# Kernel tuning notes

Hardware: AMD Instinct MI355X
Metric: run time of the kernel (lower is better)

The kernel has to match this reference:

```python
import jax, jax.numpy as jnp
import numpy as np

E = 8          # moe_expert_count
CAPACITY = 1024  # per-expert capacity C = S / E (capacity factor 1)


def _top1_gate(features, wg):
    """Top-1 gate with capacity, returning combine_weights [S,E,C],
    dispatch_mask [S,E,C], and load-balancing aux loss (standard Switch/BASE-style gate
    matching the (l_aux, combine_weights, dispatch_mask) interface used by BaseLayer)."""
    S, M = features.shape
    logits = features @ wg                      # [S, E]
    gates = jax.nn.softmax(logits, axis=-1)     # [S, E]
    idx = jnp.argmax(gates, axis=-1)            # [S] expert assignment
    mask1 = jax.nn.one_hot(idx, E, dtype=features.dtype)  # [S, E]
    # position of each token inside its expert's buffer (0-based, order of arrival)
    locations = jnp.cumsum(mask1, axis=0) - mask1          # [S, E]
    loc = jnp.sum(locations * mask1, axis=1).astype(jnp.int32)  # [S]
    keep = (loc < CAPACITY).astype(features.dtype)          # drop overflow tokens
    mask1 = mask1 * keep[:, None]
    gate_s = jnp.sum(gates * mask1, axis=1)                 # [S] gate prob of kept tokens
    loc_oh = jax.nn.one_hot(loc, CAPACITY, dtype=features.dtype)  # [S, C]
    combine = gate_s[:, None, None] * mask1[:, :, None] * loc_oh[:, None, :]  # [S,E,C]
    dispatch = (combine > 0).astype(features.dtype)
    # load-balance aux loss: E * sum(mean_prob_e * frac_tokens_e)
    me = jnp.mean(gates, axis=0)
    ce = jnp.mean(mask1, axis=0)
    l_aux = jnp.sum(me * ce) * E
    return l_aux, combine, dispatch


def setup_inputs() -> dict:
    key = jax.random.key(0)
    k0, k1, k2, k3 = jax.random.split(key, 4)
    B, T, M, H = 4, 2048, 512, 1024
    return {
        "hidden_states": jax.random.normal(k0, (B, T, M), dtype=jnp.float32),
        "wg": jax.random.normal(k1, (M, E), dtype=jnp.float32) * 0.02,
        "w1": jax.random.normal(k2, (E, M, H), dtype=jnp.float32) * 0.02,
        "b1": jnp.zeros((E, H), dtype=jnp.float32),
        "w2": jax.random.normal(k3, (E, H, M), dtype=jnp.float32) * 0.02,
        "b2": jnp.zeros((E, M), dtype=jnp.float32),
    }


def reference(hidden_states, wg, w1, b1, w2, b2):
    B, T, M = hidden_states.shape
    feats = hidden_states.reshape(-1, M)            # [S, M]
    l_aux, combine, dispatch = _top1_gate(feats, wg)
    # dense one-hot dispatch matmul: (E*C, S) @ (S, M) -> [E, C, M]
    dispatched = jnp.einsum('sec,sm->ecm', dispatch, feats)
    # per-expert FFN (BaseSublayer: Linear -> ReLU -> Linear)
    h = jax.nn.relu(jnp.einsum('ecm,emh->ech', dispatched, w1) + b1[:, None, :])
    expert_out = jnp.einsum('ech,ehn->ecn', h, w2) + b2[:, None, :]  # [E, C, M]
    # dense combine matmul: (S, E*C) @ (E*C, M) -> [S, M]
    combined = jnp.einsum('sec,ecn->sn', combine, expert_out)
    return combined.reshape(B, T, -1), l_aux
```

## Files before the change

kernel.cpp:

```cpp
#include <hip/hip_runtime.h>

#define S_TOK 8192
#define M_DIM 512
#define E_NUM 8
#define CAP   1024
#define H_DIM 1024

typedef __attribute__((ext_vector_type(8))) short bf16x8;
typedef __attribute__((ext_vector_type(4))) float f32x4;

__device__ static inline unsigned short f2bf(float f) {
    unsigned int u = __float_as_uint(f);
    unsigned int r = (u + 0x7fffu + ((u >> 16) & 1u)) >> 16;
    return (unsigned short)r;
}

__device__ static inline void async_copy16(const void* g, void* l) {
    __builtin_amdgcn_global_load_lds(
        (const __attribute__((address_space(1))) void*)g,
        (__attribute__((address_space(3))) void*)l, 16, 0, 0);
}

__global__ __launch_bounds__(256) void gate_kernel(
    const float* __restrict__ feats, const float* __restrict__ wg,
    int* __restrict__ idx, float* __restrict__ gate_top,
    float* __restrict__ gates_full, unsigned short* __restrict__ xb)
{
    const int wave = threadIdx.x >> 6;
    const int lane = threadIdx.x & 63;
    const int s = blockIdx.x * 4 + wave;

    const float* xrow = feats + (size_t)s * M_DIM;

    {
        const int m0 = lane * 8;
        const float4 va = *(const float4*)(xrow + m0);
        const float4 vb = *(const float4*)(xrow + m0 + 4);
        bf16x8 o;
        o[0] = (short)f2bf(va.x); o[1] = (short)f2bf(va.y);
        o[2] = (short)f2bf(va.z); o[3] = (short)f2bf(va.w);
        o[4] = (short)f2bf(vb.x); o[5] = (short)f2bf(vb.y);
        o[6] = (short)f2bf(vb.z); o[7] = (short)f2bf(vb.w);
        *(bf16x8*)(xb + (size_t)s * M_DIM + m0) = o;
        if (blockIdx.x == 0 && wave == 0) {
            bf16x8 z = (bf16x8){0,0,0,0,0,0,0,0};
            *(bf16x8*)(xb + (size_t)S_TOK * M_DIM + m0) = z;
        }
    }

    float p[8];
#pragma unroll
    for (int e = 0; e < 8; ++e) p[e] = 0.f;

    for (int i = 0; i < M_DIM / 64; ++i) {
        const int m = lane + 64 * i;
        const float x = xrow[m];
        const float* wrow = wg + m * 8;
#pragma unroll
        for (int e = 0; e < 8; ++e) p[e] += x * wrow[e];
    }
#pragma unroll
    for (int e = 0; e < 8; ++e) {
        float v = p[e];
#pragma unroll
        for (int off = 1; off < 64; off <<= 1) v += __shfl_xor(v, off, 64);
        p[e] = v;
    }
    if (lane == 0) {
        float mx = p[0];
#pragma unroll
        for (int e = 1; e < 8; ++e) mx = fmaxf(mx, p[e]);
        float ex[8], sum = 0.f;
#pragma unroll
        for (int e = 0; e < 8; ++e) { ex[e] = expf(p[e] - mx); sum += ex[e]; }
        const float inv = 1.0f / sum;
        int best = 0; float bl = p[0];
#pragma unroll
        for (int e = 1; e < 8; ++e) { if (p[e] > bl) { bl = p[e]; best = e; } }
#pragma unroll
        for (int e = 0; e < 8; ++e) gates_full[s * 8 + e] = ex[e] * inv;
        idx[s] = best;
        gate_top[s] = ex[best] * inv;
    }
}

__global__ __launch_bounds__(256) void scan_kernel(
    const int* __restrict__ idx, const float* __restrict__ gate_top,
    const float* __restrict__ gates_full,
    float* __restrict__ gate_final, int* __restrict__ token_list,
    int* __restrict__ kept, float* __restrict__ laux,
    int* __restrict__ dropped, int* __restrict__ ndrop)
{
    __shared__ int   cnts[256][8];
    __shared__ float msum[256][8];
    __shared__ int   totals[8];
    __shared__ float mesum[8];
    __shared__ int   dropctr;

    const int t = threadIdx.x;
    const int base = t * 32;

    for (int i = t; i < E_NUM * CAP; i += 256) token_list[i] = S_TOK;
    if (t == 0) dropctr = 0;

    int   c[8];
    float g[8];
#pragma unroll
    for (int e = 0; e < 8; ++e) { c[e] = 0; g[e] = 0.f; }

    for (int i = 0; i < 32; ++i) {
        const int ei = idx[base + i];
#pragma unroll
        for (int e = 0; e < 8; ++e) c[e] += (ei == e) ? 1 : 0;
#pragma unroll
        for (int e = 0; e < 8; ++e) g[e] += gates_full[(base + i) * 8 + e];
    }
#pragma unroll
    for (int e = 0; e < 8; ++e) { cnts[t][e] = c[e]; msum[t][e] = g[e]; }
    __syncthreads();

    if (t < 8) {
        int run = 0; float ms = 0.f;
        for (int r = 0; r < 256; ++r) {
            const int v = cnts[r][t];
            cnts[r][t] = run;
            run += v;
            ms += msum[r][t];
        }
        totals[t] = run;
        mesum[t] = ms;
        kept[t] = run < CAP ? run : CAP;
    }
    __syncthreads();

    if (t == 0) {
        float l = 0.f;
        for (int e = 0; e < 8; ++e) {
            const int ke = totals[e] < CAP ? totals[e] : CAP;
            l += (mesum[e] / (float)S_TOK) * ((float)ke / (float)S_TOK);
        }
        laux[0] = l * (float)E_NUM;
    }

    int rc[8];
#pragma unroll
    for (int e = 0; e < 8; ++e) rc[e] = cnts[t][e];

    for (int i = 0; i < 32; ++i) {
        const int s = base + i;
        const int ei = idx[s];
        int loc = 0;
#pragma unroll
        for (int e = 0; e < 8; ++e) {
            if (ei == e) { loc = rc[e]; rc[e] = rc[e] + 1; }
        }
        const bool keepit = loc < CAP;
        gate_final[s] = keepit ? gate_top[s] : 0.f;
        if (keepit) {
            token_list[ei * CAP + loc] = s;
        } else {
            const int d = atomicAdd(&dropctr, 1);
            dropped[d] = s;
        }
    }
    __syncthreads();
    if (t == 0) ndrop[0] = dropctr;
}

__global__ __launch_bounds__(256) void zero_dropped(
    const int* __restrict__ dropped, const int* __restrict__ ndrop,
    float* __restrict__ out)
{
    const int n = ndrop[0];
    const int t = threadIdx.x;
    for (int d = blockIdx.x; d < n; d += gridDim.x) {
        const int s = dropped[d];
        float2 z = make_float2(0.f, 0.f);
        *(float2*)(out + (size_t)s * M_DIM + t * 2) = z;
    }
}

__global__ __launch_bounds__(256) void convert_w(
    const float* __restrict__ w1, unsigned short* __restrict__ w1t,
    const float* __restrict__ w2, unsigned short* __restrict__ w2t)
{
    __shared__ float tile[32][33];
    int b = blockIdx.x;
    const float* src; unsigned short* dst;
    int e, k0, n0, K, N;
    if (b < 4096) {
        e = b >> 9; k0 = ((b >> 5) & 15) * 32; n0 = (b & 31) * 32;
        K = 512; N = 1024; src = w1; dst = w1t;
    } else {
        b -= 4096;
        e = b >> 9; k0 = ((b >> 4) & 31) * 32; n0 = (b & 15) * 32;
        K = 1024; N = 512; src = w2; dst = w2t;
    }
    const int t = threadIdx.x;
    const int r = t >> 5, c = t & 31;
#pragma unroll
    for (int i = 0; i < 4; ++i) {
        const int row = r + i * 8;
        tile[row][c] = src[((size_t)e * K + k0 + row) * N + n0 + c];
    }
    __syncthreads();
#pragma unroll
    for (int i = 0; i < 4; ++i) {
        const int row = r + i * 8;
        dst[((size_t)e * N + n0 + row) * K + k0 + c] = f2bf(tile[c][row]);
    }
}

__global__ __launch_bounds__(256) void ffn1_mfma(
    const unsigned short* __restrict__ xb, const unsigned short* __restrict__ w1t,
    const float* __restrict__ b1, const int* __restrict__ tok,
    const int* __restrict__ kept, unsigned short* __restrict__ h)
{
    const int b = blockIdx.x;
    const int e = b & 7;
    const int r = b >> 3;
    const int ct = r >> 3, nt = r & 7;
    const int c0 = ct * 128, n0 = nt * 128;
    if (c0 >= kept[e]) return;

    __shared__ __align__(16) short Alds[128 * 64];
    __shared__ __align__(16) short Blds[128 * 64];
    __shared__ int srow[128];

    const int t = threadIdx.x;
    const int wave = t >> 6, lane = t & 63;
    const int wm = wave & 1, wn = wave >> 1;
    const int q = lane >> 4, lr = lane & 15;

    if (t < 128) srow[t] = tok[e * CAP + c0 + t];

    f32x4 acc[4][4];
#pragma unroll
    for (int mi = 0; mi < 4; ++mi)
#pragma unroll
        for (int ni = 0; ni < 4; ++ni) acc[mi][ni] = (f32x4){0.f, 0.f, 0.f, 0.f};

    for (int kb = 0; kb < M_DIM; kb += 64) {
        __syncthreads();
#pragma unroll
        for (int i = 0; i < 4; ++i) {
            const int lin = (i * 4 + wave) * 64 + lane;
            const int row = lin >> 3, ch = lin & 7;
            async_copy16(xb + (size_t)srow[row] * M_DIM + kb + ch * 8, Alds + lin * 8);
        }
#pragma unroll
        for (int i = 0; i < 4; ++i) {
            const int lin = (i * 4 + wave) * 64 + lane;
            const int row = lin >> 3, ch = lin & 7;
            async_copy16(w1t + ((size_t)e * H_DIM + n0 + row) * M_DIM + kb + ch * 8,
                         Blds + lin * 8);
        }
        __syncthreads();

#pragma unroll
        for (int kk = 0; kk < 64; kk += 32) {
            bf16x8 af[4], bfv[4];
#pragma unroll
            for (int mi = 0; mi < 4; ++mi)
                af[mi] = *(const bf16x8*)(Alds + (wm * 64 + mi * 16 + lr) * 64 + kk + q * 8);
#pragma unroll
            for (int ni = 0; ni < 4; ++ni)
                bfv[ni] = *(const bf16x8*)(Blds + (wn * 64 + ni * 16 + lr) * 64 + kk + q * 8);
#pragma unroll
            for (int mi = 0; mi < 4; ++mi)
#pragma unroll
                for (int ni = 0; ni < 4; ++ni)
                    acc[mi][ni] = __builtin_amdgcn_mfma_f32_16x16x32_bf16(
                        af[mi], bfv[ni], acc[mi][ni], 0, 0, 0);
        }
    }

#pragma unroll
    for (int ni = 0; ni < 4; ++ni) {
        const int col = n0 + wn * 64 + ni * 16 + lr;
        const float bias = b1[e * H_DIM + col];
#pragma unroll
        for (int mi = 0; mi < 4; ++mi) {
            const int rowl = wm * 64 + mi * 16 + q * 4;
            const size_t basep = (size_t)(e * CAP + c0 + rowl) * H_DIM + col;
#pragma unroll
            for (int r2 = 0; r2 < 4; ++r2) {
                const float v = fmaxf(acc[mi][ni][r2] + bias, 0.f);
                h[basep + (size_t)r2 * H_DIM] = f2bf(v);
            }
        }
    }
}

__global__ __launch_bounds__(256) void ffn2_mfma(
    const unsigned short* __restrict__ h, const unsigned short* __restrict__ w2t,
    const float* __restrict__ b2, const int* __restrict__ tok,
    const int* __restrict__ kept, const float* __restrict__ gate_final,
    float* __restrict__ out)
{
    const int b = blockIdx.x;
    const int e = b & 7;
    const int r = b >> 3;
    const int ct = r >> 3, nt = r & 7;
    const int c0 = ct * 128, n0 = nt * 64;
    if (c0 >= kept[e]) return;

    __shared__ __align__(16) short Alds[128 * 64];
    __shared__ __align__(16) short Blds[64 * 64];

    const int t = threadIdx.x;
    const int wave = t >> 6, lane = t & 63;
    const int wm = wave & 1, wn = wave >> 1;
    const int q = lane >> 4, lr = lane & 15;

    f32x4 acc[4][2];
#pragma unroll
    for (int mi = 0; mi < 4; ++mi)
#pragma unroll
        for (int ni = 0; ni < 2; ++ni) acc[mi][ni] = (f32x4){0.f, 0.f, 0.f, 0.f};

    for (int kb = 0; kb < H_DIM; kb += 64) {
        __syncthreads();
#pragma unroll
        for (int i = 0; i < 4; ++i) {
            const int lin = (i * 4 + wave) * 64 + lane;
            const int row = lin >> 3, ch = lin & 7;
            async_copy16(h + (size_t)(e * CAP + c0 + row) * H_DIM + kb + ch * 8,
                         Alds + lin * 8);
        }
#pragma unroll
        for (int i = 0; i < 2; ++i) {
            const int lin = (i * 4 + wave) * 64 + lane;
            const int row = lin >> 3, ch = lin & 7;
            async_copy16(w2t + ((size_t)e * M_DIM + n0 + row) * H_DIM + kb + ch * 8,
                         Blds + lin * 8);
        }
        __syncthreads();

#pragma unroll
        for (int kk = 0; kk < 64; kk += 32) {
            bf16x8 af[4], bfv[2];
#pragma unroll
            for (int mi = 0; mi < 4; ++mi)
                af[mi] = *(const bf16x8*)(Alds + (wm * 64 + mi * 16 + lr) * 64 + kk + q * 8);
#pragma unroll
            for (int ni = 0; ni < 2; ++ni)
                bfv[ni] = *(const bf16x8*)(Blds + (wn * 32 + ni * 16 + lr) * 64 + kk + q * 8);
#pragma unroll
            for (int mi = 0; mi < 4; ++mi)
#pragma unroll
                for (int ni = 0; ni < 2; ++ni)
                    acc[mi][ni] = __builtin_amdgcn_mfma_f32_16x16x32_bf16(
                        af[mi], bfv[ni], acc[mi][ni], 0, 0, 0);
        }
    }

#pragma unroll
    for (int ni = 0; ni < 2; ++ni) {
        const int col = n0 + wn * 32 + ni * 16 + lr;
        const float bias = b2[e * M_DIM + col];
#pragma unroll
        for (int mi = 0; mi < 4; ++mi) {
            const int rowl = wm * 64 + mi * 16 + q * 4;
#pragma unroll
            for (int r2 = 0; r2 < 4; ++r2) {
                const int slot = c0 + rowl + r2;
                const int tokid = tok[e * CAP + slot];
                if (tokid != S_TOK) {
                    const float gsc = gate_final[tokid];
                    out[(size_t)tokid * M_DIM + col] = gsc * (acc[mi][ni][r2] + bias);
                }
            }
        }
    }
}

extern "C" void kernel_launch(void* const* d_in, const int* in_sizes, int n_in,
                              void* d_out, int out_size, void* d_ws, size_t ws_size,
                              hipStream_t stream) {
    const float* feats = (const float*)d_in[0];
    const float* wg    = (const float*)d_in[1];
    const float* w1    = (const float*)d_in[2];
    const float* b1    = (const float*)d_in[3];
    const float* w2    = (const float*)d_in[4];
    const float* b2    = (const float*)d_in[5];
    float* out = (float*)d_out;

    char* ws = (char*)d_ws;
    size_t off = 0;
    unsigned short* h   = (unsigned short*)(ws + off); off += (size_t)E_NUM * CAP * H_DIM * 2;
    unsigned short* xb  = (unsigned short*)(ws + off); off += (size_t)(S_TOK + 1) * M_DIM * 2;
    unsigned short* w1t = (unsigned short*)(ws + off); off += (size_t)E_NUM * H_DIM * M_DIM * 2;
    unsigned short* w2t = (unsigned short*)(ws + off); off += (size_t)E_NUM * M_DIM * H_DIM * 2;
    int*   idx        = (int*)(ws + off);   off += (size_t)S_TOK * 4;
    float* gate_top   = (float*)(ws + off); off += (size_t)S_TOK * 4;
    float* gate_final = (float*)(ws + off); off += (size_t)S_TOK * 4;
    float* gates_full = (float*)(ws + off); off += (size_t)S_TOK * 8 * 4;
    int*   token_list = (int*)(ws + off);   off += (size_t)S_TOK * 4;
    int*   dropped    = (int*)(ws + off);   off += (size_t)S_TOK * 4;
    int*   kept       = (int*)(ws + off);   off += 64;
    int*   ndrop      = (int*)(ws + off);   off += 64;
    (void)ws_size; (void)n_in; (void)in_sizes;

    gate_kernel<<<S_TOK / 4, 256, 0, stream>>>(feats, wg, idx, gate_top,
                                               gates_full, xb);
    convert_w<<<8192, 256, 0, stream>>>(w1, w1t, w2, w2t);
    scan_kernel<<<1, 256, 0, stream>>>(idx, gate_top, gates_full, gate_final,
                                       token_list, kept, out + (size_t)S_TOK * M_DIM,
                                       dropped, ndrop);
    zero_dropped<<<256, 256, 0, stream>>>(dropped, ndrop, out);
    ffn1_mfma<<<512, 256, 0, stream>>>(xb, w1t, b1, token_list, kept, h);
    ffn2_mfma<<<512, 256, 0, stream>>>(h, w2t, b2, token_list, kept,
                                       gate_final, out);
}
```

Baseline: 193.8 us.

## Double-buffer and swizzle FFN GEMM tiles, pre-reduce gate sums, vectorize weight conversion

Both FFN MFMA kernels now double-buffer their LDS tiles, so loads for the next K block are issued before the current one is computed. The LDS layout is XOR-swizzled to cut bank conflicts on fragment reads. The gate kernel reuses the loaded row for the logits, reads wg with float4 loads, and writes per-block partial gate sums so the single-block scan reads far less data. convert_w moves to float4 loads and ushort4 stores, and ffn2 caches token ids and gate scales in shared memory. The double buffer relies on global_load_lds finishing before the next barrier and doubles LDS use, which may reduce occupancy.

```diff
diff --git a/kernel.cpp b/kernel.cpp
--- a/kernel.cpp
+++ b/kernel.cpp
@@ -5,6 +5,7 @@
 #define E_NUM 8
 #define CAP   1024
 #define H_DIM 1024
+#define NGATE_BLK (S_TOK / 4)
 
 typedef __attribute__((ext_vector_type(8))) short bf16x8;
 typedef __attribute__((ext_vector_type(4))) float f32x4;
@@ -24,23 +25,24 @@
 __global__ __launch_bounds__(256) void gate_kernel(
     const float* __restrict__ feats, const float* __restrict__ wg,
     int* __restrict__ idx, float* __restrict__ gate_top,
-    float* __restrict__ gates_full, unsigned short* __restrict__ xb)
-{
+    float* __restrict__ gates_psum, unsigned short* __restrict__ xb)
+{
+    __shared__ float gsh[4][8];
     const int wave = threadIdx.x >> 6;
     const int lane = threadIdx.x & 63;
     const int s = blockIdx.x * 4 + wave;
 
     const float* xrow = feats + (size_t)s * M_DIM;
+    const int m0 = lane * 8;
+
+    const float4 va = *(const float4*)(xrow + m0);
+    const float4 vb = *(const float4*)(xrow + m0 + 4);
+    float xv[8] = {va.x, va.y, va.z, va.w, vb.x, vb.y, vb.z, vb.w};
 
     {
-        const int m0 = lane * 8;
-        const float4 va = *(const float4*)(xrow + m0);
-        const float4 vb = *(const float4*)(xrow + m0 + 4);
         bf16x8 o;
-        o[0] = (short)f2bf(va.x); o[1] = (short)f2bf(va.y);
-        o[2] = (short)f2bf(va.z); o[3] = (short)f2bf(va.w);
-        o[4] = (short)f2bf(vb.x); o[5] = (short)f2bf(vb.y);
-        o[6] = (short)f2bf(vb.z); o[7] = (short)f2bf(vb.w);
+#pragma unroll
+        for (int j = 0; j < 8; ++j) o[j] = (short)f2bf(xv[j]);
         *(bf16x8*)(xb + (size_t)s * M_DIM + m0) = o;
         if (blockIdx.x == 0 && wave == 0) {
             bf16x8 z = (bf16x8){0,0,0,0,0,0,0,0};
@@ -51,13 +53,13 @@
     float p[8];
 #pragma unroll
     for (int e = 0; e < 8; ++e) p[e] = 0.f;
-
-    for (int i = 0; i < M_DIM / 64; ++i) {
-        const int m = lane + 64 * i;
-        const float x = xrow[m];
-        const float* wrow = wg + m * 8;
-#pragma unroll
-        for (int e = 0; e < 8; ++e) p[e] += x * wrow[e];
+#pragma unroll
+    for (int j = 0; j < 8; ++j) {
+        const float4 wa = *(const float4*)(wg + (m0 + j) * 8);
+        const float4 wb2 = *(const float4*)(wg + (m0 + j) * 8 + 4);
+        const float x = xv[j];
+        p[0] += x * wa.x;  p[1] += x * wa.y;  p[2] += x * wa.z;  p[3] += x * wa.w;
+        p[4] += x * wb2.x; p[5] += x * wb2.y; p[6] += x * wb2.z; p[7] += x * wb2.w;
     }
 #pragma unroll
     for (int e = 0; e < 8; ++e) {
@@ -78,15 +80,21 @@
 #pragma unroll
         for (int e = 1; e < 8; ++e) { if (p[e] > bl) { bl = p[e]; best = e; } }
 #pragma unroll
-        for (int e = 0; e < 8; ++e) gates_full[s * 8 + e] = ex[e] * inv;
+        for (int e = 0; e < 8; ++e) gsh[wave][e] = ex[e] * inv;
         idx[s] = best;
         gate_top[s] = ex[best] * inv;
     }
+    __syncthreads();
+    if (threadIdx.x < 8) {
+        const int e = threadIdx.x;
+        gates_psum[blockIdx.x * 8 + e] =
+            gsh[0][e] + gsh[1][e] + gsh[2][e] + gsh[3][e];
+    }
 }
 
 __global__ __launch_bounds__(256) void scan_kernel(
     const int* __restrict__ idx, const float* __restrict__ gate_top,
-    const float* __restrict__ gates_full,
+    const float* __restrict__ gates_psum,
     float* __restrict__ gate_final, int* __restrict__ token_list,
     int* __restrict__ kept, float* __restrict__ laux,
     int* __restrict__ dropped, int* __restrict__ ndrop)
@@ -103,17 +111,24 @@
     for (int i = t; i < E_NUM * CAP; i += 256) token_list[i] = S_TOK;
     if (t == 0) dropctr = 0;
 
-    int   c[8];
-    float g[8];
-#pragma unroll
-    for (int e = 0; e < 8; ++e) { c[e] = 0; g[e] = 0.f; }
-
+    int c[8];
+#pragma unroll
+    for (int e = 0; e < 8; ++e) c[e] = 0;
     for (int i = 0; i < 32; ++i) {
         const int ei = idx[base + i];
 #pragma unroll
         for (int e = 0; e < 8; ++e) c[e] += (ei == e) ? 1 : 0;
-#pragma unroll
-        for (int e = 0; e < 8; ++e) g[e] += gates_full[(base + i) * 8 + e];
+    }
+
+    float g[8];
+#pragma unroll
+    for (int e = 0; e < 8; ++e) g[e] = 0.f;
+    for (int i = 0; i < NGATE_BLK / 256; ++i) {
+        const float* gp = gates_psum + (size_t)(t + 256 * i) * 8;
+        const float4 a = *(const float4*)gp;
+        const float4 b = *(const float4*)(gp + 4);
+        g[0] += a.x; g[1] += a.y; g[2] += a.z; g[3] += a.w;
+        g[4] += b.x; g[5] += b.y; g[6] += b.z; g[7] += b.w;
     }
 #pragma unroll
     for (int e = 0; e < 8; ++e) { cnts[t][e] = c[e]; msum[t][e] = g[e]; }
@@ -175,8 +190,7 @@
     const int t = threadIdx.x;
     for (int d = blockIdx.x; d < n; d += gridDim.x) {
         const int s = dropped[d];
-        float2 z = make_float2(0.f, 0.f);
-        *(float2*)(out + (size_t)s * M_DIM + t * 2) = z;
+        *(float2*)(out + (size_t)s * M_DIM + t * 2) = make_float2(0.f, 0.f);
     }
 }
 
@@ -197,17 +211,18 @@
         K = 1024; N = 512; src = w2; dst = w2t;
     }
     const int t = threadIdx.x;
-    const int r = t >> 5, c = t & 31;
-#pragma unroll
-    for (int i = 0; i < 4; ++i) {
-        const int row = r + i * 8;
-        tile[row][c] = src[((size_t)e * K + k0 + row) * N + n0 + c];
-    }
-    __syncthreads();
-#pragma unroll
-    for (int i = 0; i < 4; ++i) {
-        const int row = r + i * 8;
-        dst[((size_t)e * N + n0 + row) * K + k0 + c] = f2bf(tile[c][row]);
+    const int r = t >> 3, c4 = (t & 7) * 4;
+    {
+        const float4 v = *(const float4*)(src + ((size_t)e * K + k0 + r) * N + n0 + c4);
+        tile[r][c4 + 0] = v.x; tile[r][c4 + 1] = v.y;
+        tile[r][c4 + 2] = v.z; tile[r][c4 + 3] = v.w;
+    }
+    __syncthreads();
+    {
+        ushort4 o;
+        o.x = f2bf(tile[c4 + 0][r]); o.y = f2bf(tile[c4 + 1][r]);
+        o.z = f2bf(tile[c4 + 2][r]); o.w = f2bf(tile[c4 + 3][r]);
+        *(ushort4*)(dst + ((size_t)e * N + n0 + r) * K + k0 + c4) = o;
     }
 }
 
@@ -223,8 +238,8 @@
     const int c0 = ct * 128, n0 = nt * 128;
     if (c0 >= kept[e]) return;
 
-    __shared__ __align__(16) short Alds[128 * 64];
-    __shared__ __align__(16) short Blds[128 * 64];
+    __shared__ __align__(16) short Alds[2][128 * 64];
+    __shared__ __align__(16) short Blds[2][128 * 64];
     __shared__ int srow[128];
 
     const int t = threadIdx.x;
@@ -234,38 +249,53 @@
 
     if (t < 128) srow[t] = tok[e * CAP + c0 + t];
 
+    auto stage = [&](int buf, int kb) {
+#pragma unroll
+        for (int i = 0; i < 4; ++i) {
+            const int lin = (i * 4 + wave) * 64 + lane;
+            const int row = lin >> 3;
+            const int ch = (lin & 7) ^ (row & 7);
+            async_copy16(xb + (size_t)srow[row] * M_DIM + kb + ch * 8,
+                         &Alds[buf][lin * 8]);
+        }
+#pragma unroll
+        for (int i = 0; i < 4; ++i) {
+            const int lin = (i * 4 + wave) * 64 + lane;
+            const int row = lin >> 3;
+            const int ch = (lin & 7) ^ (row & 7);
+            async_copy16(w1t + ((size_t)e * H_DIM + n0 + row) * M_DIM + kb + ch * 8,
+                         &Blds[buf][lin * 8]);
+        }
+    };
+
     f32x4 acc[4][4];
 #pragma unroll
     for (int mi = 0; mi < 4; ++mi)
 #pragma unroll
         for (int ni = 0; ni < 4; ++ni) acc[mi][ni] = (f32x4){0.f, 0.f, 0.f, 0.f};
 
+    __syncthreads();
+    stage(0, 0);
+
+    int cur = 0;
     for (int kb = 0; kb < M_DIM; kb += 64) {
         __syncthreads();
-#pragma unroll
-        for (int i = 0; i < 4; ++i) {
-            const int lin = (i * 4 + wave) * 64 + lane;
-            const int row = lin >> 3, ch = lin & 7;
-            async_copy16(xb + (size_t)srow[row] * M_DIM + kb + ch * 8, Alds + lin * 8);
-        }
-#pragma unroll
-        for (int i = 0; i < 4; ++i) {
-            const int lin = (i * 4 + wave) * 64 + lane;
-            const int row = lin >> 3, ch = lin & 7;
-            async_copy16(w1t + ((size_t)e * H_DIM + n0 + row) * M_DIM + kb + ch * 8,
-                         Blds + lin * 8);
-        }
-        __syncthreads();
+        if (kb + 64 < M_DIM) stage(cur ^ 1, kb + 64);
 
 #pragma unroll
         for (int kk = 0; kk < 64; kk += 32) {
+            const int cb = kk >> 3;
             bf16x8 af[4], bfv[4];
 #pragma unroll
-            for (int mi = 0; mi < 4; ++mi)
-                af[mi] = *(const bf16x8*)(Alds + (wm * 64 + mi * 16 + lr) * 64 + kk + q * 8);
-#pragma unroll
-            for (int ni = 0; ni < 4; ++ni)
-                bfv[ni] = *(const bf16x8*)(Blds + (wn * 64 + ni * 16 + lr) * 64 + kk + q * 8);
+            for (int mi = 0; mi < 4; ++mi) {
+                const int R = wm * 64 + mi * 16 + lr;
+                af[mi] = *(const bf16x8*)(&Alds[cur][(R * 8 + ((cb + q) ^ (R & 7))) * 8]);
+            }
+#pragma unroll
+            for (int ni = 0; ni < 4; ++ni) {
+                const int R = wn * 64 + ni * 16 + lr;
+                bfv[ni] = *(const bf16x8*)(&Blds[cur][(R * 8 + ((cb + q) ^ (R & 7))) * 8]);
+            }
 #pragma unroll
             for (int mi = 0; mi < 4; ++mi)
 #pragma unroll
@@ -273,6 +303,7 @@
                     acc[mi][ni] = __builtin_amdgcn_mfma_f32_16x16x32_bf16(
                         af[mi], bfv[ni], acc[mi][ni], 0, 0, 0);
         }
+        cur ^= 1;
     }
 
 #pragma unroll
@@ -305,47 +336,69 @@
     const int c0 = ct * 128, n0 = nt * 64;
     if (c0 >= kept[e]) return;
 
-    __shared__ __align__(16) short Alds[128 * 64];
-    __shared__ __align__(16) short Blds[64 * 64];
+    __shared__ __align__(16) short Alds[2][128 * 64];
+    __shared__ __align__(16) short Blds[2][64 * 64];
+    __shared__ int   stok[128];
+    __shared__ float sgf[128];
 
     const int t = threadIdx.x;
     const int wave = t >> 6, lane = t & 63;
     const int wm = wave & 1, wn = wave >> 1;
     const int q = lane >> 4, lr = lane & 15;
 
+    if (t < 128) {
+        const int tk = tok[e * CAP + c0 + t];
+        stok[t] = tk;
+        sgf[t] = (tk != S_TOK) ? gate_final[tk] : 0.f;
+    }
+
+    auto stage = [&](int buf, int kb) {
+#pragma unroll
+        for (int i = 0; i < 4; ++i) {
+            const int lin = (i * 4 + wave) * 64 + lane;
+            const int row = lin >> 3;
+            const int ch = (lin & 7) ^ (row & 7);
+            async_copy16(h + (size_t)(e * CAP + c0 + row) * H_DIM + kb + ch * 8,
+                         &Alds[buf][lin * 8]);
+        }
+#pragma unroll
+        for (int i = 0; i < 2; ++i) {
+            const int lin = (i * 4 + wave) * 64 + lane;
+            const int row = lin >> 3;
+            const int ch = (lin & 7) ^ (row & 7);
+            async_copy16(w2t + ((size_t)e * M_DIM + n0 + row) * H_DIM + kb + ch * 8,
+                         &Blds[buf][lin * 8]);
+        }
+    };
+
     f32x4 acc[4][2];
 #pragma unroll
     for (int mi = 0; mi < 4; ++mi)
 #pragma unroll
         for (int ni = 0; ni < 2; ++ni) acc[mi][ni] = (f32x4){0.f, 0.f, 0.f, 0.f};
 
+    __syncthreads();
+    stage(0, 0);
+
+    int cur = 0;
     for (int kb = 0; kb < H_DIM; kb += 64) {
         __syncthreads();
-#pragma unroll
-        for (int i = 0; i < 4; ++i) {
-            const int lin = (i * 4 + wave) * 64 + lane;
-            const int row = lin >> 3, ch = lin & 7;
-            async_copy16(h + (size_t)(e * CAP + c0 + row) * H_DIM + kb + ch * 8,
-                         Alds + lin * 8);
-        }
-#pragma unroll
-        for (int i = 0; i < 2; ++i) {
-            const int lin = (i * 4 + wave) * 64 + lane;
-            const int row = lin >> 3, ch = lin & 7;
-            async_copy16(w2t + ((size_t)e * M_DIM + n0 + row) * H_DIM + kb + ch * 8,
-                         Blds + lin * 8);
-        }
-        __syncthreads();
+        if (kb + 64 < H_DIM) stage(cur ^ 1, kb + 64);
 
 #pragma unroll
         for (int kk = 0; kk < 64; kk += 32) {
+            const int cb = kk >> 3;
             bf16x8 af[4], bfv[2];
 #pragma unroll
-            for (int mi = 0; mi < 4; ++mi)
-                af[mi] = *(const bf16x8*)(Alds + (wm * 64 + mi * 16 + lr) * 64 + kk + q * 8);
-#pragma unroll
-            for (int ni = 0; ni < 2; ++ni)
-                bfv[ni] = *(const bf16x8*)(Blds + (wn * 32 + ni * 16 + lr) * 64 + kk + q * 8);
+            for (int mi = 0; mi < 4; ++mi) {
+                const int R = wm * 64 + mi * 16 + lr;
+                af[mi] = *(const bf16x8*)(&Alds[cur][(R * 8 + ((cb + q) ^ (R & 7))) * 8]);
+            }
+#pragma unroll
+            for (int ni = 0; ni < 2; ++ni) {
+                const int R = wn * 32 + ni * 16 + lr;
+                bfv[ni] = *(const bf16x8*)(&Blds[cur][(R * 8 + ((cb + q) ^ (R & 7))) * 8]);
+            }
 #pragma unroll
             for (int mi = 0; mi < 4; ++mi)
 #pragma unroll
@@ -353,6 +406,7 @@
                     acc[mi][ni] = __builtin_amdgcn_mfma_f32_16x16x32_bf16(
                         af[mi], bfv[ni], acc[mi][ni], 0, 0, 0);
         }
+        cur ^= 1;
     }
 
 #pragma unroll
@@ -364,11 +418,10 @@
             const int rowl = wm * 64 + mi * 16 + q * 4;
 #pragma unroll
             for (int r2 = 0; r2 < 4; ++r2) {
-                const int slot = c0 + rowl + r2;
-                const int tokid = tok[e * CAP + slot];
+                const int slot = rowl + r2;
+                const int tokid = stok[slot];
                 if (tokid != S_TOK) {
-                    const float gsc = gate_final[tokid];
-                    out[(size_t)tokid * M_DIM + col] = gsc * (acc[mi][ni][r2] + bias);
+                    out[(size_t)tokid * M_DIM + col] = sgf[slot] * (acc[mi][ni][r2] + bias);
                 }
             }
         }
@@ -395,17 +448,17 @@
     int*   idx        = (int*)(ws + off);   off += (size_t)S_TOK * 4;
     float* gate_top   = (float*)(ws + off); off += (size_t)S_TOK * 4;
     float* gate_final = (float*)(ws + off); off += (size_t)S_TOK * 4;
-    float* gates_full = (float*)(ws + off); off += (size_t)S_TOK * 8 * 4;
+    float* gates_psum = (float*)(ws + off); off += (size_t)NGATE_BLK * 8 * 4;
     int*   token_list = (int*)(ws + off);   off += (size_t)S_TOK * 4;
     int*   dropped    = (int*)(ws + off);   off += (size_t)S_TOK * 4;
     int*   kept       = (int*)(ws + off);   off += 64;
     int*   ndrop      = (int*)(ws + off);   off += 64;
     (void)ws_size; (void)n_in; (void)in_sizes;
 
-    gate_kernel<<<S_TOK / 4, 256, 0, stream>>>(feats, wg, idx, gate_top,
-                                               gates_full, xb);
+    gate_kernel<<<NGATE_BLK, 256, 0, stream>>>(feats, wg, idx, gate_top,
+                                               gates_psum, xb);
     convert_w<<<8192, 256, 0, stream>>>(w1, w1t, w2, w2t);
-    scan_kernel<<<1, 256, 0, stream>>>(idx, gate_top, gates_full, gate_final,
+    scan_kernel<<<1, 256, 0, stream>>>(idx, gate_top, gates_psum, gate_final,
                                        token_list, kept, out + (size_t)S_TOK * M_DIM,
                                        dropped, ndrop);
     zero_dropped<<<256, 256, 0, stream>>>(dropped, ndrop, out);
```

Result: faster. 186.1 us (-4.0%).
